# Kernel optimization log

Hardware: AMD Instinct MI355X
Metric: run time of the kernel (lower is better)

## Reference

```python
import jax, jax.numpy as jnp
import numpy as np

N_NODES = 100000
N_EDGES = 1600000
D_INPUT = 128
D_HIDDEN = 16
N_HEADS = 8
NCLASSES = 40
N_GRAPHS = 64
ALPHA = 0.2  # LeakyReLU negative slope
INIT = 0.01  # GAT_param_init uniform range


def setup_inputs() -> dict:
    key = jax.random.key(0)
    ks = jax.random.split(key, 7)
    x = jax.random.normal(ks[0], (N_NODES, D_INPUT), dtype=jnp.float32)
    edge_idx = jax.random.randint(ks[1], (2, N_EDGES), 0, N_NODES, dtype=jnp.int64)
    batch = jnp.sort(jax.random.randint(ks[2], (N_NODES,), 0, N_GRAPHS, dtype=jnp.int64))
    # layer1: d_input -> n_heads * d_hidden, concat aggregate
    W1 = jax.random.uniform(ks[3], (D_INPUT, N_HEADS * D_HIDDEN), dtype=jnp.float32, minval=-INIT, maxval=INIT)
    a1 = jax.random.uniform(ks[4], (N_HEADS, 2 * D_HIDDEN), dtype=jnp.float32, minval=-INIT, maxval=INIT)
    # layer2: n_heads*d_hidden -> nclasses, 1 head, mean aggregate
    W2 = jax.random.uniform(ks[5], (N_HEADS * D_HIDDEN, NCLASSES), dtype=jnp.float32, minval=-INIT, maxval=INIT)
    a2 = jax.random.uniform(ks[6], (1, 2 * NCLASSES), dtype=jnp.float32, minval=-INIT, maxval=INIT)
    return {"x": x, "W1": W1, "a1": a1, "W2": W2, "a2": a2, "edge_idx": edge_idx, "batch": batch}


def _gat_layer(x, W, a, n_heads, d_out, src, dst, aggregate):
    # x: [N, d_in]; W: [d_in, H*D]; a: [H, 2*D]
    n = x.shape[0]
    Wh = (x @ W).reshape(n, n_heads, d_out)                  # [N, H, D]
    e_src = jnp.einsum('nhd,hd->nh', Wh, a[:, :d_out])       # [N, H]
    e_dst = jnp.einsum('nhd,hd->nh', Wh, a[:, d_out:])       # [N, H]
    e = jax.nn.leaky_relu(e_src[src] + e_dst[dst], ALPHA)    # [E, H]
    # segment softmax over edges sharing the same destination node
    m = jax.ops.segment_max(e, dst, num_segments=n)          # [N, H]
    m = jnp.where(jnp.isfinite(m), m, 0.0)                   # nodes w/o in-edges
    ex = jnp.exp(e - m[dst])
    s = jax.ops.segment_sum(ex, dst, num_segments=n)
    att = ex / (s[dst] + 1e-16)                              # [E, H]
    # weighted scatter-aggregate of neighbor features
    out = jax.ops.segment_sum(att[:, :, None] * Wh[src], dst, num_segments=n)  # [N, H, D]
    if aggregate == 'concat':
        return out.reshape(n, n_heads * d_out)
    return out.mean(axis=1)


def reference(x, W1, a1, W2, a2, edge_idx, batch):
    # eval mode: F.dropout(training=False) is identity
    src, dst = edge_idx[0], edge_idx[1]
    h1 = _gat_layer(x, W1, a1, N_HEADS, D_HIDDEN, src, dst, 'concat')
    h1 = jax.nn.elu(h1)
    h2 = _gat_layer(h1, W2, a2, 1, NCLASSES, src, dst, 'mean')   # [N, nclasses]
    # global_mean_pool over graph ids
    sums = jax.ops.segment_sum(h2, batch, num_segments=N_GRAPHS)
    cnt = jax.ops.segment_sum(jnp.ones((h2.shape[0],), h2.dtype), batch, num_segments=N_GRAPHS)
    return sums / jnp.maximum(cnt, 1.0)[:, None]
```

## Files before the change

### kernel.cpp

```cpp
#include <hip/hip_runtime.h>
#include <hip/hip_bf16.h>

typedef unsigned short u16;
typedef unsigned int   u32;
typedef float f32x2 __attribute__((ext_vector_type(2)));

static constexpr int NN = 100000;
static constexpr int NE = 1600000;
static constexpr int NG = 64;

static constexpr int BSH   = 8;
static constexpr int NBUCK = 391;
static constexpr int BCAP  = 5120;
static constexpr int PB    = 8;

__device__ __forceinline__ u32 bf16pair(float a, float b) {
  u32 ua = __builtin_bit_cast(u32, a), ub = __builtin_bit_cast(u32, b);
  ua = (ua + 0x7FFFu + ((ua >> 16) & 1u)) >> 16;
  ub = (ub + 0x7FFFu + ((ub >> 16) & 1u)) >> 16;
  return ua | (ub << 16);
}
__device__ __forceinline__ float bflo(u32 u) { return __builtin_bit_cast(float, u << 16); }
__device__ __forceinline__ float bfhi(u32 u) { return __builtin_bit_cast(float, u & 0xFFFF0000u); }

__device__ __forceinline__ void pkfma(f32x2& a, f32x2 w2, u32 u) {
  f32x2 v;
  v.x = bflo(u); v.y = bfhi(u);
  asm("v_pk_fma_f32 %0, %1, %2, %0" : "+v"(a) : "v"(w2), "v"(v));
}

__global__ __launch_bounds__(256) void k_gemm1(
    const float* __restrict__ x, const float* __restrict__ W1,
    const float* __restrict__ a1,
    u16* __restrict__ Wh1b, float* __restrict__ es1, float* __restrict__ ed1)
{
  __shared__ float xs[64][36];
  __shared__ float ws[32][128];
  const int t = threadIdx.x;
  const int rowBase = blockIdx.x * 64;
  const int r0 = (t >> 4) * 4;
  const int c0 = (t & 15) * 8;
  float acc[4][8];
#pragma unroll
  for (int r = 0; r < 4; ++r)
#pragma unroll
    for (int c = 0; c < 8; ++c) acc[r][c] = 0.f;

  for (int k0 = 0; k0 < 128; k0 += 32) {
#pragma unroll
    for (int p = 0; p < 2; ++p) {
      int rr = (t >> 3) + p * 32;
      int cc = (t & 7) * 4;
      int grow = rowBase + rr;
      float4 v = make_float4(0.f, 0.f, 0.f, 0.f);
      if (grow < NN) v = *(const float4*)(&x[(size_t)grow * 128 + k0 + cc]);
      *(float4*)(&xs[rr][cc]) = v;
    }
#pragma unroll
    for (int p = 0; p < 4; ++p) {
      int idx = (p * 256 + t) * 4;
      int kk = idx >> 7, cc = idx & 127;
      *(float4*)(&ws[kk][cc]) = *(const float4*)(&W1[(size_t)(k0 + kk) * 128 + cc]);
    }
    __syncthreads();
#pragma unroll
    for (int k = 0; k < 32; ++k) {
      float a[4], b[8];
#pragma unroll
      for (int r = 0; r < 4; ++r) a[r] = xs[r0 + r][k];
      *(float4*)&b[0] = *(float4*)&ws[k][c0];
      *(float4*)&b[4] = *(float4*)&ws[k][c0 + 4];
#pragma unroll
      for (int r = 0; r < 4; ++r)
#pragma unroll
        for (int c = 0; c < 8; ++c) acc[r][c] = fmaf(a[r], b[c], acc[r][c]);
    }
    __syncthreads();
  }
  const int h = (t & 15) >> 1;
  const int dbase = (t & 1) * 8;
  float a1s[8], a1d[8];
#pragma unroll
  for (int j = 0; j < 8; ++j) {
    a1s[j] = a1[h * 32 + dbase + j];
    a1d[j] = a1[h * 32 + 16 + dbase + j];
  }
#pragma unroll
  for (int r = 0; r < 4; ++r) {
    int grow = rowBase + r0 + r;
    float pes = 0.f, ped = 0.f;
#pragma unroll
    for (int j = 0; j < 8; ++j) {
      pes = fmaf(acc[r][j], a1s[j], pes);
      ped = fmaf(acc[r][j], a1d[j], ped);
    }
    pes += __shfl_xor(pes, 1);
    ped += __shfl_xor(ped, 1);
    if (grow < NN) {
      u32 p0 = bf16pair(acc[r][0], acc[r][1]);
      u32 p1 = bf16pair(acc[r][2], acc[r][3]);
      u32 p2 = bf16pair(acc[r][4], acc[r][5]);
      u32 p3 = bf16pair(acc[r][6], acc[r][7]);
      *(uint4*)(Wh1b + (size_t)grow * 128 + c0) = make_uint4(p0, p1, p2, p3);
      if ((t & 1) == 0) { es1[grow * 8 + h] = pes; ed1[grow * 8 + h] = ped; }
    }
  }
}

__global__ __launch_bounds__(256) void k_bin(
    const int* __restrict__ src, const int* __restrict__ dst,
    int* __restrict__ cur, u32* __restrict__ ebuf)
{
  __shared__ int lcnt[512];
  __shared__ int goff[NBUCK];
  __shared__ u32 bin[4096];
  const int t = threadIdx.x;
  const int e0 = blockIdx.x * 4096;

  lcnt[t] = 0; lcnt[t + 256] = 0;
  __syncthreads();

  u32 ent[16]; short bb[16], lp[16];
#pragma unroll
  for (int i = 0; i < 16; ++i) {
    int e = e0 + i * 256 + t;
    if (e < NE) {
      int s = src[e], d = dst[e];
      int b = d >> BSH;
      ent[i] = (u32)s | ((u32)(d & 255) << 20);
      bb[i] = (short)b;
      lp[i] = (short)atomicAdd(&lcnt[b], 1);
    } else bb[i] = -1;
  }
  __syncthreads();
  for (int d = 1; d < 512; d <<= 1) {
    int v0 = (t >= d) ? lcnt[t - d] : 0;
    int v1 = (t + 256 >= d) ? lcnt[t + 256 - d] : 0;
    __syncthreads();
    lcnt[t] += v0; lcnt[t + 256] += v1;
    __syncthreads();
  }
  for (int b = t; b < NBUCK; b += 256) {
    int excl = b ? lcnt[b - 1] : 0;
    int cnt = lcnt[b] - excl;
    if (cnt) goff[b] = b * BCAP + atomicAdd(&cur[b], cnt);
  }
#pragma unroll
  for (int i = 0; i < 16; ++i) {
    if (bb[i] >= 0) {
      int excl = bb[i] ? lcnt[bb[i] - 1] : 0;
      bin[excl + lp[i]] = ent[i];
    }
  }
  __syncthreads();
  const int total = lcnt[NBUCK - 1];
  for (int i = t; i < total; i += 256) {
    int lo = 0, hi = NBUCK - 1;
    while (lo < hi) { int mid = (lo + hi) >> 1; if (lcnt[mid] > i) hi = mid; else lo = mid + 1; }
    int excl = lo ? lcnt[lo - 1] : 0;
    int g = goff[lo] + (i - excl);
    if (g < (lo + 1) * BCAP) ebuf[g] = bin[i];
  }
}

__global__ __launch_bounds__(256) void k_sort(
    const int* __restrict__ cur, u32* __restrict__ ebuf,
    int* __restrict__ offs, int* __restrict__ deg)
{
  __shared__ u32 ein[BCAP];
  __shared__ u32 eout[BCAP];
  __shared__ int nd[256];
  __shared__ int ncur[256];
  const int t = threadIdx.x;
  const int b = blockIdx.x;
  const int base = b * BCAP;
  int cnt = cur[b];
  if (cnt > BCAP) cnt = BCAP;
  const int nloc = min(256, NN - (b << BSH));

  for (int i = t; i < cnt; i += 256) ein[i] = ebuf[base + i];
  nd[t] = 0;
  __syncthreads();
  for (int i = t; i < cnt; i += 256) atomicAdd(&nd[ein[i] >> 20], 1);
  __syncthreads();
  const int myCnt = nd[t];
  for (int d = 1; d < 256; d <<= 1) {
    int v = (t >= d) ? nd[t - d] : 0;
    __syncthreads();
    nd[t] += v;
    __syncthreads();
  }
  const int excl = t ? nd[t - 1] : 0;
  ncur[t] = excl;
  if (t < nloc) {
    int node = (b << BSH) + t;
    offs[node] = base + excl;
    deg[node]  = myCnt;
  }
  __syncthreads();
  for (int i = t; i < cnt; i += 256) {
    u32 v = ein[i];
    int pos = atomicAdd(&ncur[v >> 20], 1);
    eout[pos] = v & 0xFFFFFu;
  }
  __syncthreads();
  for (int i = t; i < cnt; i += 256) ebuf[base + i] = eout[i];
}

__global__ __launch_bounds__(256) void k_agg1(
    const u16* __restrict__ Wh1b, const float* __restrict__ es1, const float* __restrict__ ed1,
    const int* __restrict__ offs, const int* __restrict__ deg, const int* __restrict__ csr,
    u16* __restrict__ h1b)
{
  const int wid = threadIdx.x >> 6;
  const int lane = threadIdx.x & 63;
  const int n = blockIdx.x * 4 + wid;
  if (n >= NN) return;
  const int s0 = offs[n];
  const int nE = deg[n];
  const int g = lane >> 4;
  const int db = lane & 15;
  const int h = db >> 1;
  const float edv = ed1[n * 8 + h];

  f32x2 acc[4];
#pragma unroll
  for (int i = 0; i < 4; ++i) { acc[i].x = 0.f; acc[i].y = 0.f; }
  float ssum = 0.f;

  for (int c0 = 0; c0 < nE; c0 += 8) {
    const int j0 = c0 + g;
    const int j1 = c0 + 4 + g;
    const int sA = csr[s0 + (j0 < nE ? j0 : 0)];
    const int sB = csr[s0 + (j1 < nE ? j1 : 0)];
    float zA = es1[sA * 8 + h] + edv;
    float zB = es1[sB * 8 + h] + edv;
    zA = (zA > 0.f) ? zA : 0.2f * zA;
    zB = (zB > 0.f) ? zB : 0.2f * zB;
    if (j0 < nE) {
      const uint4 raw = *(const uint4*)(Wh1b + (size_t)sA * 128 + db * 8);
      const float w = __expf(zA);
      ssum += w;
      f32x2 w2; w2.x = w; w2.y = w;
      pkfma(acc[0], w2, raw.x);
      pkfma(acc[1], w2, raw.y);
      pkfma(acc[2], w2, raw.z);
      pkfma(acc[3], w2, raw.w);
    }
    if (j1 < nE) {
      const uint4 raw = *(const uint4*)(Wh1b + (size_t)sB * 128 + db * 8);
      const float w = __expf(zB);
      ssum += w;
      f32x2 w2; w2.x = w; w2.y = w;
      pkfma(acc[0], w2, raw.x);
      pkfma(acc[1], w2, raw.y);
      pkfma(acc[2], w2, raw.z);
      pkfma(acc[3], w2, raw.w);
    }
  }
#pragma unroll
  for (int i = 0; i < 4; ++i) {
    acc[i].x += __shfl_xor(acc[i].x, 16);
    acc[i].y += __shfl_xor(acc[i].y, 16);
    acc[i].x += __shfl_xor(acc[i].x, 32);
    acc[i].y += __shfl_xor(acc[i].y, 32);
  }
  ssum += __shfl_xor(ssum, 16);
  ssum += __shfl_xor(ssum, 32);

  if (g == 0) {
    float inv = 1.f / (ssum + 1e-16f);
    float o[8];
#pragma unroll
    for (int i = 0; i < 4; ++i) {
      float v0 = acc[i].x * inv;
      float v1 = acc[i].y * inv;
      o[2 * i]     = (v0 > 0.f) ? v0 : expm1f(v0);
      o[2 * i + 1] = (v1 > 0.f) ? v1 : expm1f(v1);
    }
    u32 p0 = bf16pair(o[0], o[1]);
    u32 p1 = bf16pair(o[2], o[3]);
    u32 p2 = bf16pair(o[4], o[5]);
    u32 p3 = bf16pair(o[6], o[7]);
    *(uint4*)(h1b + (size_t)n * 128 + db * 8) = make_uint4(p0, p1, p2, p3);
  }
}

__global__ __launch_bounds__(256) void k_gemm2(
    const u16* __restrict__ h1b, const float* __restrict__ W2,
    const float* __restrict__ a2,
    u16* __restrict__ Wh2b, float* __restrict__ es2, float* __restrict__ ed2)
{
  __shared__ float hs[128][36];
  __shared__ float w2s[32][40];
  const int t = threadIdx.x;
  const int rowBase = blockIdx.x * 128;
  const int cg = t & 3;
  const int rs = t >> 2;
  float acc[2][10];
#pragma unroll
  for (int r = 0; r < 2; ++r)
#pragma unroll
    for (int j = 0; j < 10; ++j) acc[r][j] = 0.f;

  for (int k0 = 0; k0 < 128; k0 += 32) {
#pragma unroll
    for (int p = 0; p < 2; ++p) {
      int idx = (p * 256 + t) * 8;
      int rr = idx >> 5, cc = idx & 31;
      int grow = rowBase + rr;
      uint4 hv = make_uint4(0u, 0u, 0u, 0u);
      if (grow < NN) hv = *(const uint4*)(h1b + (size_t)grow * 128 + k0 + cc);
      float2* dst = (float2*)&hs[rr][cc];
      dst[0] = make_float2(bflo(hv.x), bfhi(hv.x));
      dst[1] = make_float2(bflo(hv.y), bfhi(hv.y));
      dst[2] = make_float2(bflo(hv.z), bfhi(hv.z));
      dst[3] = make_float2(bflo(hv.w), bfhi(hv.w));
    }
#pragma unroll
    for (int p = 0; p < 5; ++p) {
      int idx = p * 256 + t;
      int kk = idx / 40, cc = idx % 40;
      w2s[kk][cc] = W2[(size_t)(k0 + kk) * 40 + cc];
    }
    __syncthreads();
#pragma unroll
    for (int k = 0; k < 32; ++k) {
      float a0 = hs[rs][k], a1v = hs[rs + 64][k];
#pragma unroll
      for (int j = 0; j < 10; ++j) {
        float b = w2s[k][cg * 10 + j];
        acc[0][j] = fmaf(a0, b, acc[0][j]);
        acc[1][j] = fmaf(a1v, b, acc[1][j]);
      }
    }
    __syncthreads();
  }
  float a2s[10], a2d[10];
#pragma unroll
  for (int j = 0; j < 10; ++j) {
    a2s[j] = a2[cg * 10 + j];
    a2d[j] = a2[40 + cg * 10 + j];
  }
#pragma unroll
  for (int rr = 0; rr < 2; ++rr) {
    int grow = rowBase + rs + rr * 64;
    float pes = 0.f, ped = 0.f;
#pragma unroll
    for (int j = 0; j < 10; ++j) {
      float v = acc[rr][j];
      pes = fmaf(v, a2s[j], pes);
      ped = fmaf(v, a2d[j], ped);
    }
    if (grow < NN) {
      u32* dst = (u32*)(Wh2b + (size_t)grow * 48 + cg * 10);
      dst[0] = bf16pair(acc[rr][0], acc[rr][1]);
      dst[1] = bf16pair(acc[rr][2], acc[rr][3]);
      dst[2] = bf16pair(acc[rr][4], acc[rr][5]);
      dst[3] = bf16pair(acc[rr][6], acc[rr][7]);
      dst[4] = bf16pair(acc[rr][8], acc[rr][9]);
    }
    pes += __shfl_xor(pes, 1); pes += __shfl_xor(pes, 2);
    ped += __shfl_xor(ped, 1); ped += __shfl_xor(ped, 2);
    if (cg == 0 && grow < NN) { es2[grow] = pes; ed2[grow] = ped; }
  }
}

__global__ __launch_bounds__(256) void k_agg2(
    const u16* __restrict__ Wh2b, const float* __restrict__ es2, const float* __restrict__ ed2,
    const int* __restrict__ offs, const int* __restrict__ deg, const int* __restrict__ csr,
    float* __restrict__ h2)
{
  __shared__ float red[4][64][9];
  const int wid = threadIdx.x >> 6;
  const int lane = threadIdx.x & 63;
  const int n = blockIdx.x * 4 + wid;
  if (n >= NN) return;
  const int s0 = offs[n];
  const int nE = deg[n];
  const float edv = ed2[n];
  const int e5 = lane / 5, r5 = lane - e5 * 5;
  const bool act = lane < 60;

  f32x2 acc[4];
#pragma unroll
  for (int i = 0; i < 4; ++i) { acc[i].x = 0.f; acc[i].y = 0.f; }
  float ssum = 0.f;

  for (int c0 = 0; c0 < nE; c0 += 24) {
    const int j0 = c0 + e5;
    const int j1 = c0 + 12 + e5;
    const int sA = csr[s0 + (j0 < nE ? j0 : 0)];
    const int sB = csr[s0 + (j1 < nE ? j1 : 0)];
    float zA = es2[sA] + edv;
    float zB = es2[sB] + edv;
    zA = (zA > 0.f) ? zA : 0.2f * zA;
    zB = (zB > 0.f) ? zB : 0.2f * zB;
    if (act && j0 < nE) {
      const uint4 raw = *(const uint4*)(Wh2b + (size_t)sA * 48 + r5 * 8);
      const float w = __expf(zA);
      ssum += w;
      f32x2 w2; w2.x = w; w2.y = w;
      pkfma(acc[0], w2, raw.x);
      pkfma(acc[1], w2, raw.y);
      pkfma(acc[2], w2, raw.z);
      pkfma(acc[3], w2, raw.w);
    }
    if (act && j1 < nE) {
      const uint4 raw = *(const uint4*)(Wh2b + (size_t)sB * 48 + r5 * 8);
      const float w = __expf(zB);
      ssum += w;
      f32x2 w2; w2.x = w; w2.y = w;
      pkfma(acc[0], w2, raw.x);
      pkfma(acc[1], w2, raw.y);
      pkfma(acc[2], w2, raw.z);
      pkfma(acc[3], w2, raw.w);
    }
  }
#pragma unroll
  for (int i = 0; i < 4; ++i) {
    red[wid][lane][2 * i]     = acc[i].x;
    red[wid][lane][2 * i + 1] = acc[i].y;
  }
  red[wid][lane][8] = ssum;
  __builtin_amdgcn_wave_barrier();
  if (lane < 40) {
    int slot = lane >> 3, i = lane & 7;
    float a = 0.f, sm = 0.f;
#pragma unroll
    for (int g = 0; g < 12; ++g) {
      a  += red[wid][g * 5 + slot][i];
      sm += red[wid][g * 5][8];
    }
    h2[(size_t)n * 40 + lane] = a / (sm + 1e-16f);
  }
}

__global__ void k_gbounds(const int* __restrict__ batch, int* __restrict__ gstart) {
  int g = threadIdx.x;
  if (g > NG) return;
  int lo = 0, hi = NN;
  while (lo < hi) { int mid = (lo + hi) >> 1; if (batch[mid] < g) lo = mid + 1; else hi = mid; }
  gstart[g] = lo;
}

__global__ __launch_bounds__(256) void k_pool1(
    const float* __restrict__ h2, const int* __restrict__ gstart,
    float* __restrict__ partial)
{
  __shared__ float lds[25][10][4];
  const int g = blockIdx.x >> 3;
  const int p = blockIdx.x & 7;
  const int t = threadIdx.x;
  const int s0 = gstart[g], s1 = gstart[g + 1];
  const int len = s1 - s0;
  const int chunk = (len + PB - 1) / PB;
  const int start = s0 + p * chunk;
  const int end = min(start + chunk, s1);
  const int slot = t / 10, q = t - slot * 10;
  float4 acc = make_float4(0.f, 0.f, 0.f, 0.f);
  if (slot < 25) {
    for (int n = start + slot; n < end; n += 25) {
      const float4 v = *(const float4*)(&h2[(size_t)n * 40 + q * 4]);
      acc.x += v.x; acc.y += v.y; acc.z += v.z; acc.w += v.w;
    }
    lds[slot][q][0] = acc.x; lds[slot][q][1] = acc.y;
    lds[slot][q][2] = acc.z; lds[slot][q][3] = acc.w;
  }
  __syncthreads();
  if (t < 40) {
    const int qq = t >> 2, e = t & 3;
    float s = 0.f;
#pragma unroll
    for (int sl = 0; sl < 25; ++sl) s += lds[sl][qq][e];
    partial[(size_t)blockIdx.x * 40 + t] = s;
  }
}

__global__ void k_pool2(const float* __restrict__ partial, const int* __restrict__ gstart,
                        float* __restrict__ out)
{
  const int g = blockIdx.x;
  const int d = threadIdx.x;
  if (d >= 40) return;
  float s = 0.f;
#pragma unroll
  for (int p = 0; p < PB; ++p) s += partial[(size_t)(g * PB + p) * 40 + d];
  int cnt = gstart[g + 1] - gstart[g];
  if (cnt < 1) cnt = 1;
  out[g * 40 + d] = s / (float)cnt;
}

extern "C" void kernel_launch(void* const* d_in, const int* in_sizes, int n_in,
                              void* d_out, int out_size, void* d_ws, size_t ws_size,
                              hipStream_t stream)
{
  const float* x   = (const float*)d_in[0];
  const float* W1  = (const float*)d_in[1];
  const float* a1  = (const float*)d_in[2];
  const float* W2  = (const float*)d_in[3];
  const float* a2  = (const float*)d_in[4];
  const int* eidx  = (const int*)d_in[5];
  const int* batch = (const int*)d_in[6];
  float* out = (float*)d_out;

  char* ws = (char*)d_ws;
  u16*   Wh1b = (u16*)(ws + 0);
  u16*   Wh2b = (u16*)(ws + 0);
  float* h2   = (float*)(ws + 9600000);
  u16*   h1b  = (u16*)(ws + 25600000);
  float* es1  = (float*)(ws + 51200000);
  float* ed1  = (float*)(ws + 54400000);
  float* es2  = (float*)(ws + 57600000);
  float* ed2  = (float*)(ws + 58000000);
  u32*   ebuf = (u32*)(ws + 58400000);
  int*   offs = (int*)(ws + 66407680);
  int*   deg  = (int*)(ws + 66807680);
  int*   cur  = (int*)(ws + 67207680);
  int*   gstart = (int*)(ws + 67209728);
  float* partial = (float*)(ws + 67210240);

  const int* esrc = eidx;
  const int* edst = eidx + NE;

  hipMemsetAsync(cur, 0, NBUCK * sizeof(int), stream);
  k_gbounds<<<1, 128, 0, stream>>>(batch, gstart);
  k_gemm1<<<(NN + 63) / 64, 256, 0, stream>>>(x, W1, a1, Wh1b, es1, ed1);
  k_bin<<<(NE + 4095) / 4096, 256, 0, stream>>>(esrc, edst, cur, ebuf);
  k_sort<<<NBUCK, 256, 0, stream>>>(cur, ebuf, offs, deg);
  k_agg1<<<(NN + 3) / 4, 256, 0, stream>>>(Wh1b, es1, ed1, offs, deg, (const int*)ebuf, h1b);
  k_gemm2<<<(NN + 127) / 128, 256, 0, stream>>>(h1b, W2, a2, Wh2b, es2, ed2);
  k_agg2<<<(NN + 3) / 4, 256, 0, stream>>>(Wh2b, es2, ed2, offs, deg, (const int*)ebuf, h2);
  k_pool1<<<NG * PB, 256, 0, stream>>>(h2, gstart, partial);
  k_pool2<<<NG, 64, 0, stream>>>(partial, gstart, out);
}
```

Measured before the change: 286.3 us.

## Use bf16 MFMA for layer-1 GEMM and batch edge loads in aggregation

The first-layer projection now runs on bf16 MFMA instructions instead of scalar fp32 FMAs. A new prep kernel transposes W1, converts it to bf16 with a swizzle, and the GEMM stages x into LDS as swizzled bf16. Separately, the layer-1 aggregation loop is unrolled to issue 16 edges' gather loads together, which raises memory-level parallelism. The trade-offs are extra rounding of x and W1 to bf16, per-element scalar stores of Wh1b, and an added kernel launch.

```diff
diff --git a/kernel.cpp b/kernel.cpp
--- a/kernel.cpp
+++ b/kernel.cpp
@@ -4,6 +4,8 @@
 typedef unsigned short u16;
 typedef unsigned int   u32;
 typedef float f32x2 __attribute__((ext_vector_type(2)));
+typedef float f32x4 __attribute__((ext_vector_type(4)));
+typedef short bf16x8 __attribute__((ext_vector_type(8)));
 
 static constexpr int NN = 100000;
 static constexpr int NE = 1600000;
@@ -14,11 +16,13 @@
 static constexpr int BCAP  = 5120;
 static constexpr int PB    = 8;
 
+__device__ __forceinline__ u16 bf16rte(float a) {
+  u32 u = __builtin_bit_cast(u32, a);
+  u = (u + 0x7FFFu + ((u >> 16) & 1u)) >> 16;
+  return (u16)u;
+}
 __device__ __forceinline__ u32 bf16pair(float a, float b) {
-  u32 ua = __builtin_bit_cast(u32, a), ub = __builtin_bit_cast(u32, b);
-  ua = (ua + 0x7FFFu + ((ua >> 16) & 1u)) >> 16;
-  ub = (ub + 0x7FFFu + ((ub >> 16) & 1u)) >> 16;
-  return ua | (ub << 16);
+  return (u32)bf16rte(a) | ((u32)bf16rte(b) << 16);
 }
 __device__ __forceinline__ float bflo(u32 u) { return __builtin_bit_cast(float, u << 16); }
 __device__ __forceinline__ float bfhi(u32 u) { return __builtin_bit_cast(float, u & 0xFFFF0000u); }
@@ -29,80 +33,101 @@
   asm("v_pk_fma_f32 %0, %1, %2, %0" : "+v"(a) : "v"(w2), "v"(v));
 }
 
+__global__ void k_prepW(const float* __restrict__ W1, u16* __restrict__ wsTg) {
+  const int t = threadIdx.x;
+  for (int rep = 0; rep < 64; ++rep) {
+    int idx = rep * 256 + t;
+    int k = idx >> 7, c = idx & 127;
+    float v = W1[idx];
+    wsTg[c * 128 + (((k >> 3) ^ (c & 7)) << 3) + (k & 7)] = bf16rte(v);
+  }
+}
+
 __global__ __launch_bounds__(256) void k_gemm1(
-    const float* __restrict__ x, const float* __restrict__ W1,
-    const float* __restrict__ a1,
+    const float* __restrict__ x, const u16* __restrict__ wsTg, const float* __restrict__ a1,
     u16* __restrict__ Wh1b, float* __restrict__ es1, float* __restrict__ ed1)
 {
-  __shared__ float xs[64][36];
-  __shared__ float ws[32][128];
+  __shared__ u16 wsT[128][128];
+  __shared__ u16 xsb[64][32];
   const int t = threadIdx.x;
+  const int w = t >> 6, l = t & 63;
   const int rowBase = blockIdx.x * 64;
-  const int r0 = (t >> 4) * 4;
-  const int c0 = (t & 15) * 8;
-  float acc[4][8];
+
+  {
+    const uint4* src = (const uint4*)wsTg;
+    uint4* dst = (uint4*)&wsT[0][0];
+#pragma unroll
+    for (int i = 0; i < 8; ++i) dst[t * 8 + i] = src[t * 8 + i];
+  }
+
+  f32x4 acc[4][2];
 #pragma unroll
   for (int r = 0; r < 4; ++r)
 #pragma unroll
-    for (int c = 0; c < 8; ++c) acc[r][c] = 0.f;
-
-  for (int k0 = 0; k0 < 128; k0 += 32) {
-#pragma unroll
-    for (int p = 0; p < 2; ++p) {
-      int rr = (t >> 3) + p * 32;
-      int cc = (t & 7) * 4;
-      int grow = rowBase + rr;
-      float4 v = make_float4(0.f, 0.f, 0.f, 0.f);
-      if (grow < NN) v = *(const float4*)(&x[(size_t)grow * 128 + k0 + cc]);
-      *(float4*)(&xs[rr][cc]) = v;
-    }
-#pragma unroll
-    for (int p = 0; p < 4; ++p) {
-      int idx = (p * 256 + t) * 4;
-      int kk = idx >> 7, cc = idx & 127;
-      *(float4*)(&ws[kk][cc]) = *(const float4*)(&W1[(size_t)(k0 + kk) * 128 + cc]);
-    }
-    __syncthreads();
-#pragma unroll
-    for (int k = 0; k < 32; ++k) {
-      float a[4], b[8];
-#pragma unroll
-      for (int r = 0; r < 4; ++r) a[r] = xs[r0 + r][k];
-      *(float4*)&b[0] = *(float4*)&ws[k][c0];
-      *(float4*)&b[4] = *(float4*)&ws[k][c0 + 4];
-#pragma unroll
-      for (int r = 0; r < 4; ++r)
-#pragma unroll
-        for (int c = 0; c < 8; ++c) acc[r][c] = fmaf(a[r], b[c], acc[r][c]);
-    }
-    __syncthreads();
-  }
-  const int h = (t & 15) >> 1;
-  const int dbase = (t & 1) * 8;
-  float a1s[8], a1d[8];
-#pragma unroll
-  for (int j = 0; j < 8; ++j) {
-    a1s[j] = a1[h * 32 + dbase + j];
-    a1d[j] = a1[h * 32 + 16 + dbase + j];
-  }
-#pragma unroll
-  for (int r = 0; r < 4; ++r) {
-    int grow = rowBase + r0 + r;
-    float pes = 0.f, ped = 0.f;
-#pragma unroll
-    for (int j = 0; j < 8; ++j) {
-      pes = fmaf(acc[r][j], a1s[j], pes);
-      ped = fmaf(acc[r][j], a1d[j], ped);
-    }
-    pes += __shfl_xor(pes, 1);
-    ped += __shfl_xor(ped, 1);
-    if (grow < NN) {
-      u32 p0 = bf16pair(acc[r][0], acc[r][1]);
-      u32 p1 = bf16pair(acc[r][2], acc[r][3]);
-      u32 p2 = bf16pair(acc[r][4], acc[r][5]);
-      u32 p3 = bf16pair(acc[r][6], acc[r][7]);
-      *(uint4*)(Wh1b + (size_t)grow * 128 + c0) = make_uint4(p0, p1, p2, p3);
-      if ((t & 1) == 0) { es1[grow * 8 + h] = pes; ed1[grow * 8 + h] = ped; }
+    for (int cf = 0; cf < 2; ++cf) acc[r][cf] = (f32x4){0.f, 0.f, 0.f, 0.f};
+
+  const int rr = t >> 2, cg = t & 3;
+  const int grow_s = rowBase + rr;
+
+  for (int kk0 = 0; kk0 < 128; kk0 += 32) {
+    float4 v0 = make_float4(0.f, 0.f, 0.f, 0.f), v1 = v0;
+    if (grow_s < NN) {
+      v0 = *(const float4*)(&x[(size_t)grow_s * 128 + kk0 + cg * 8]);
+      v1 = *(const float4*)(&x[(size_t)grow_s * 128 + kk0 + cg * 8 + 4]);
+    }
+    if (kk0) __syncthreads();
+    {
+      u32 p0 = bf16pair(v0.x, v0.y);
+      u32 p1 = bf16pair(v0.z, v0.w);
+      u32 p2 = bf16pair(v1.x, v1.y);
+      u32 p3 = bf16pair(v1.z, v1.w);
+      int sg = cg ^ ((rr >> 1) & 3);
+      *(uint4*)(&xsb[rr][sg * 8]) = make_uint4(p0, p1, p2, p3);
+    }
+    __syncthreads();
+
+    bf16x8 bfr[2];
+#pragma unroll
+    for (int cf = 0; cf < 2; ++cf) {
+      int col = w * 32 + cf * 16 + (l & 15);
+      int kg = (kk0 >> 3) + (l >> 4);
+      bfr[cf] = *(const bf16x8*)(&wsT[col][(kg ^ (col & 7)) * 8]);
+    }
+#pragma unroll
+    for (int r = 0; r < 4; ++r) {
+      int row = r * 16 + (l & 15);
+      int kg = l >> 4;
+      bf16x8 afr = *(const bf16x8*)(&xsb[row][(kg ^ ((row >> 1) & 3)) * 8]);
+#pragma unroll
+      for (int cf = 0; cf < 2; ++cf)
+        acc[r][cf] = __builtin_amdgcn_mfma_f32_16x16x32_bf16(afr, bfr[cf], acc[r][cf], 0, 0, 0);
+    }
+  }
+
+  const int cl = l & 15;
+  const int rq = l >> 4;
+#pragma unroll
+  for (int cf = 0; cf < 2; ++cf) {
+    const int h = w * 2 + cf;
+    const int gcol = w * 32 + cf * 16 + cl;
+    const float as = a1[h * 32 + cl];
+    const float ad = a1[h * 32 + 16 + cl];
+#pragma unroll
+    for (int r = 0; r < 4; ++r) {
+#pragma unroll
+      for (int i = 0; i < 4; ++i) {
+        int grow = rowBase + r * 16 + rq * 4 + i;
+        float wh = acc[r][cf][i];
+        float ps = wh * as, pd = wh * ad;
+        ps += __shfl_xor(ps, 1); ps += __shfl_xor(ps, 2);
+        ps += __shfl_xor(ps, 4); ps += __shfl_xor(ps, 8);
+        pd += __shfl_xor(pd, 1); pd += __shfl_xor(pd, 2);
+        pd += __shfl_xor(pd, 4); pd += __shfl_xor(pd, 8);
+        if (grow < NN) {
+          Wh1b[(size_t)grow * 128 + gcol] = bf16rte(wh);
+          if (cl == 0) { es1[grow * 8 + h] = ps; ed1[grow * 8 + h] = pd; }
+        }
+      }
     }
   }
 }
@@ -228,34 +253,57 @@
   for (int i = 0; i < 4; ++i) { acc[i].x = 0.f; acc[i].y = 0.f; }
   float ssum = 0.f;
 
-  for (int c0 = 0; c0 < nE; c0 += 8) {
-    const int j0 = c0 + g;
-    const int j1 = c0 + 4 + g;
-    const int sA = csr[s0 + (j0 < nE ? j0 : 0)];
-    const int sB = csr[s0 + (j1 < nE ? j1 : 0)];
-    float zA = es1[sA * 8 + h] + edv;
-    float zB = es1[sB * 8 + h] + edv;
-    zA = (zA > 0.f) ? zA : 0.2f * zA;
-    zB = (zB > 0.f) ? zB : 0.2f * zB;
-    if (j0 < nE) {
-      const uint4 raw = *(const uint4*)(Wh1b + (size_t)sA * 128 + db * 8);
-      const float w = __expf(zA);
-      ssum += w;
-      f32x2 w2; w2.x = w; w2.y = w;
-      pkfma(acc[0], w2, raw.x);
-      pkfma(acc[1], w2, raw.y);
-      pkfma(acc[2], w2, raw.z);
-      pkfma(acc[3], w2, raw.w);
-    }
-    if (j1 < nE) {
-      const uint4 raw = *(const uint4*)(Wh1b + (size_t)sB * 128 + db * 8);
-      const float w = __expf(zB);
-      ssum += w;
-      f32x2 w2; w2.x = w; w2.y = w;
-      pkfma(acc[0], w2, raw.x);
-      pkfma(acc[1], w2, raw.y);
-      pkfma(acc[2], w2, raw.z);
-      pkfma(acc[3], w2, raw.w);
+  int c0 = 0;
+  for (; c0 + 16 <= nE; c0 += 16) {
+    int ss[4];
+#pragma unroll
+    for (int q = 0; q < 4; ++q) ss[q] = csr[s0 + c0 + q * 4 + g];
+    float zz[4];
+#pragma unroll
+    for (int q = 0; q < 4; ++q) {
+      float z = es1[ss[q] * 8 + h] + edv;
+      zz[q] = (z > 0.f) ? z : 0.2f * z;
+    }
+    uint4 raw[4];
+#pragma unroll
+    for (int q = 0; q < 4; ++q)
+      raw[q] = *(const uint4*)(Wh1b + (size_t)ss[q] * 128 + db * 8);
+#pragma unroll
+    for (int q = 0; q < 4; ++q) {
+      const float ww = __expf(zz[q]);
+      ssum += ww;
+      f32x2 w2; w2.x = ww; w2.y = ww;
+      pkfma(acc[0], w2, raw[q].x);
+      pkfma(acc[1], w2, raw[q].y);
+      pkfma(acc[2], w2, raw[q].z);
+      pkfma(acc[3], w2, raw[q].w);
+    }
+  }
+  if (c0 < nE) {
+    int jj[4], ss[4];
+#pragma unroll
+    for (int q = 0; q < 4; ++q) {
+      jj[q] = c0 + q * 4 + g;
+      ss[q] = csr[s0 + (jj[q] < nE ? jj[q] : 0)];
+    }
+    float zz[4];
+#pragma unroll
+    for (int q = 0; q < 4; ++q) {
+      float z = es1[ss[q] * 8 + h] + edv;
+      zz[q] = (z > 0.f) ? z : 0.2f * z;
+    }
+#pragma unroll
+    for (int q = 0; q < 4; ++q) {
+      if (jj[q] < nE) {
+        const uint4 raw = *(const uint4*)(Wh1b + (size_t)ss[q] * 128 + db * 8);
+        const float ww = __expf(zz[q]);
+        ssum += ww;
+        f32x2 w2; w2.x = ww; w2.y = ww;
+        pkfma(acc[0], w2, raw.x);
+        pkfma(acc[1], w2, raw.y);
+        pkfma(acc[2], w2, raw.z);
+        pkfma(acc[3], w2, raw.w);
+      }
     }
   }
 #pragma unroll
@@ -519,13 +567,15 @@
   int*   cur  = (int*)(ws + 67207680);
   int*   gstart = (int*)(ws + 67209728);
   float* partial = (float*)(ws + 67210240);
+  u16*   wsTg = (u16*)(ws + 67292160);
 
   const int* esrc = eidx;
   const int* edst = eidx + NE;
 
   hipMemsetAsync(cur, 0, NBUCK * sizeof(int), stream);
+  k_prepW<<<1, 256, 0, stream>>>(W1, wsTg);
   k_gbounds<<<1, 128, 0, stream>>>(batch, gstart);
-  k_gemm1<<<(NN + 63) / 64, 256, 0, stream>>>(x, W1, a1, Wh1b, es1, ed1);
+  k_gemm1<<<(NN + 63) / 64, 256, 0, stream>>>(x, wsTg, a1, Wh1b, es1, ed1);
   k_bin<<<(NE + 4095) / 4096, 256, 0, stream>>>(esrc, edst, cur, ebuf);
   k_sort<<<NBUCK, 256, 0, stream>>>(cur, ebuf, offs, deg);
   k_agg1<<<(NN + 3) / 4, 256, 0, stream>>>(Wh1b, es1, ed1, offs, deg, (const int*)ebuf, h1b);
```

New measurement: 266.9 us. -6.8%, faster.
